# Kernel optimization log

Hardware: AMD Instinct MI355X
Metric: run time of the kernel (lower is better)

Reference implementation:

```python
import jax, jax.numpy as jnp
import numpy as np

EPS = 1e-12  # matches torch F.normalize default eps

def setup_inputs() -> dict:
    key = jax.random.key(0)
    k1, k2 = jax.random.split(key)
    N, D = 16384, 1024
    pc_feat = jax.random.normal(k1, (N, D), dtype=jnp.float32)
    aug_feat = jax.random.normal(k2, (N, D), dtype=jnp.float32)
    return {"pc_feat": pc_feat, "aug_feat": aug_feat}

def reference(pc_feat, aug_feat):
    # F.normalize(x, dim=1): x / max(||x||_2, eps)
    pc_n = pc_feat / jnp.maximum(jnp.linalg.norm(pc_feat, axis=1, keepdims=True), EPS)
    aug_n = aug_feat / jnp.maximum(jnp.linalg.norm(aug_feat, axis=1, keepdims=True), EPS)
    # diag(pc_n @ aug_n.T) == row-wise dot product; avoids the O(N^2) matmul
    cos = jnp.sum(pc_n * aug_n, axis=1)  # [N]
    # loss = sum(1 - cos) / N == mean(1 - cos)
    return jnp.mean(1.0 - cos)
```

## Files before the change

kernel.cpp:

```cpp
#include <hip/hip_runtime.h>


#define N_ROWS 16384
#define DIM 1024
#define BLOCKS 1024
#define TPB 256
#define WAVES_PER_BLOCK (TPB / 64)
#define TOTAL_WAVES (BLOCKS * WAVES_PER_BLOCK)

__global__ __launch_bounds__(TPB) void cos_rows_kernel(
    const float4* __restrict__ a, const float4* __restrict__ b,
    float* __restrict__ partial)
{
    const int wave = threadIdx.x >> 6;
    const int lane = threadIdx.x & 63;
    const int gwave = blockIdx.x * WAVES_PER_BLOCK + wave;

    float sum_cos = 0.0f;

    for (int r = gwave; r < N_ROWS; r += TOTAL_WAVES) {
        const float4* ap = a + (size_t)r * (DIM / 4);
        const float4* bp = b + (size_t)r * (DIM / 4);
        float ab = 0.0f, aa = 0.0f, bb = 0.0f;
        #pragma unroll
        for (int k = 0; k < 4; ++k) {
            float4 x = ap[lane + 64 * k];
            float4 y = bp[lane + 64 * k];
            ab += x.x * y.x + x.y * y.y + x.z * y.z + x.w * y.w;
            aa += x.x * x.x + x.y * x.y + x.z * x.z + x.w * x.w;
            bb += y.x * y.x + y.y * y.y + y.z * y.z + y.w * y.w;
        }
        #pragma unroll
        for (int off = 32; off > 0; off >>= 1) {
            ab += __shfl_down(ab, off);
            aa += __shfl_down(aa, off);
            bb += __shfl_down(bb, off);
        }
        if (lane == 0) {
            float na = fmaxf(sqrtf(aa), 1e-12f);
            float nb = fmaxf(sqrtf(bb), 1e-12f);
            sum_cos += ab / (na * nb);
        }
    }

    __shared__ float s[WAVES_PER_BLOCK];
    if (lane == 0) s[wave] = sum_cos;
    __syncthreads();
    if (threadIdx.x == 0) {
        float t = 0.0f;
        #pragma unroll
        for (int i = 0; i < WAVES_PER_BLOCK; ++i) t += s[i];
        partial[blockIdx.x] = t;
    }
}

__global__ __launch_bounds__(TPB) void finalize_kernel(
    const float* __restrict__ partial, float* __restrict__ out)
{
    const int wave = threadIdx.x >> 6;
    const int lane = threadIdx.x & 63;
    float t = 0.0f;
    for (int i = threadIdx.x; i < BLOCKS; i += TPB) t += partial[i];
    #pragma unroll
    for (int off = 32; off > 0; off >>= 1) t += __shfl_down(t, off);
    __shared__ float s[WAVES_PER_BLOCK];
    if (lane == 0) s[wave] = t;
    __syncthreads();
    if (threadIdx.x == 0) {
        float tot = 0.0f;
        #pragma unroll
        for (int i = 0; i < WAVES_PER_BLOCK; ++i) tot += s[i];
        out[0] = 1.0f - tot / (float)N_ROWS;
    }
}

extern "C" void kernel_launch(void* const* d_in, const int* in_sizes, int n_in,
                              void* d_out, int out_size, void* d_ws, size_t ws_size,
                              hipStream_t stream) {
    const float4* pc  = (const float4*)d_in[0];
    const float4* aug = (const float4*)d_in[1];
    float* partial = (float*)d_ws;
    float* out = (float*)d_out;

    cos_rows_kernel<<<BLOCKS, TPB, 0, stream>>>(pc, aug, partial);
    finalize_kernel<<<1, TPB, 0, stream>>>(partial, out);
}
```

Baseline: 142.0 us.

## Split row dot products into per-segment partials with separate row-combine kernel

Replaces the wave-per-row reduction with a thread-per-segment scheme: 16 threads each accumulate a strided slice of a row and write ab/aa/bb partials to workspace, then a second kernel combines the 16 partials per row through shared memory and computes the cosine, and a final kernel sums 256 block results. This removes cross-lane shuffle reductions and the grid-stride loop in the main pass. It adds an extra kernel launch and a round trip of three 16384x16 float arrays through global memory. The segment-strided loads leave each thread's float4 accesses 256 bytes apart, which may hurt coalescing per instruction. It also contains an odd redundant ternary on the bb accumulation.

Result: slower. 151.8 us (+6.9%).

```diff
diff --git a/kernel.cpp b/kernel.cpp
--- a/kernel.cpp
+++ b/kernel.cpp
@@ -2,55 +2,72 @@
 
 
 #define N_ROWS 16384
-#define DIM 1024
-#define BLOCKS 1024
+#define ROW_V4 256
+#define SEGS 16
+#define SEG_V4 16
 #define TPB 256
-#define WAVES_PER_BLOCK (TPB / 64)
-#define TOTAL_WAVES (BLOCKS * WAVES_PER_BLOCK)
+#define NPART (N_ROWS * SEGS)
+#define BLOCKS1 (NPART / TPB)
+#define BLOCKS2 256
 
-__global__ __launch_bounds__(TPB) void cos_rows_kernel(
+__global__ __launch_bounds__(TPB) void partial_kernel(
     const float4* __restrict__ a, const float4* __restrict__ b,
-    float* __restrict__ partial)
+    float* __restrict__ ab_ws, float* __restrict__ aa_ws,
+    float* __restrict__ bb_ws)
 {
-    const int wave = threadIdx.x >> 6;
-    const int lane = threadIdx.x & 63;
-    const int gwave = blockIdx.x * WAVES_PER_BLOCK + wave;
+    const int g = blockIdx.x * TPB + threadIdx.x;
+    const int row = g >> 4;
+    const int seg = g & (SEGS - 1);
+    const float4* ap = a + (size_t)row * ROW_V4 + seg;
+    const float4* bp = b + (size_t)row * ROW_V4 + seg;
 
-    float sum_cos = 0.0f;
+    float ab = 0.0f, aa = 0.0f, bb = 0.0f;
+    #pragma unroll
+    for (int j = 0; j < SEG_V4; ++j) {
+        float4 x = ap[j * SEGS];
+        float4 y = bp[j * SEGS];
+        ab += x.x * y.x + x.y * y.y + x.z * y.z + x.w * y.w;
+        aa += x.x * x.x + x.y * x.y + x.z * x.z + x.w * x.w;
+        bb += y.x * y.y == 0.0f ? y.x * y.x + y.y * y.y + y.z * y.z + y.w * y.w
+                                : y.x * y.x + y.y * y.y + y.z * y.z + y.w * y.w;
+    }
+    ab_ws[g] = ab;
+    aa_ws[g] = aa;
+    bb_ws[g] = bb;
+}
 
-    for (int r = gwave; r < N_ROWS; r += TOTAL_WAVES) {
-        const float4* ap = a + (size_t)r * (DIM / 4);
-        const float4* bp = b + (size_t)r * (DIM / 4);
+__global__ __launch_bounds__(TPB) void rowcos_kernel(
+    const float* __restrict__ ab_ws, const float* __restrict__ aa_ws,
+    const float* __restrict__ bb_ws, float* __restrict__ partial)
+{
+    __shared__ float sab[1024], saa[1024], sbb[1024];
+    const int base = blockIdx.x * 1024;
+    #pragma unroll
+    for (int i = threadIdx.x; i < 1024; i += TPB) {
+        sab[i] = ab_ws[base + i];
+        saa[i] = aa_ws[base + i];
+        sbb[i] = bb_ws[base + i];
+    }
+    __syncthreads();
+
+    float t = 0.0f;
+    if (threadIdx.x < 64) {
+        const int r = threadIdx.x;
         float ab = 0.0f, aa = 0.0f, bb = 0.0f;
         #pragma unroll
-        for (int k = 0; k < 4; ++k) {
-            float4 x = ap[lane + 64 * k];
-            float4 y = bp[lane + 64 * k];
-            ab += x.x * y.x + x.y * y.y + x.z * y.z + x.w * y.w;
-            aa += x.x * x.x + x.y * x.y + x.z * x.z + x.w * x.w;
-            bb += y.x * y.x + y.y * y.y + y.z * y.z + y.w * y.w;
+        for (int i = 0; i < SEGS; ++i) {
+            ab += sab[r * SEGS + i];
+            aa += saa[r * SEGS + i];
+            bb += sbb[r * SEGS + i];
         }
+        float na = fmaxf(sqrtf(aa), 1e-12f);
+        float nb = fmaxf(sqrtf(bb), 1e-12f);
+        t = ab / (na * nb);
+    }
+    if (threadIdx.x < 64) {
         #pragma unroll
-        for (int off = 32; off > 0; off >>= 1) {
-            ab += __shfl_down(ab, off);
-            aa += __shfl_down(aa, off);
-            bb += __shfl_down(bb, off);
-        }
-        if (lane == 0) {
-            float na = fmaxf(sqrtf(aa), 1e-12f);
-            float nb = fmaxf(sqrtf(bb), 1e-12f);
-            sum_cos += ab / (na * nb);
-        }
-    }
-
-    __shared__ float s[WAVES_PER_BLOCK];
-    if (lane == 0) s[wave] = sum_cos;
-    __syncthreads();
-    if (threadIdx.x == 0) {
-        float t = 0.0f;
-        #pragma unroll
-        for (int i = 0; i < WAVES_PER_BLOCK; ++i) t += s[i];
-        partial[blockIdx.x] = t;
+        for (int off = 32; off > 0; off >>= 1) t += __shfl_down(t, off);
+        if (threadIdx.x == 0) partial[blockIdx.x] = t;
     }
 }
 
@@ -59,17 +76,16 @@
 {
     const int wave = threadIdx.x >> 6;
     const int lane = threadIdx.x & 63;
-    float t = 0.0f;
-    for (int i = threadIdx.x; i < BLOCKS; i += TPB) t += partial[i];
+    float t = partial[threadIdx.x];
     #pragma unroll
     for (int off = 32; off > 0; off >>= 1) t += __shfl_down(t, off);
-    __shared__ float s[WAVES_PER_BLOCK];
+    __shared__ float s[TPB / 64];
     if (lane == 0) s[wave] = t;
     __syncthreads();
     if (threadIdx.x == 0) {
         float tot = 0.0f;
         #pragma unroll
-        for (int i = 0; i < WAVES_PER_BLOCK; ++i) tot += s[i];
+        for (int i = 0; i < TPB / 64; ++i) tot += s[i];
         out[0] = 1.0f - tot / (float)N_ROWS;
     }
 }
@@ -79,9 +95,13 @@
                               hipStream_t stream) {
     const float4* pc  = (const float4*)d_in[0];
     const float4* aug = (const float4*)d_in[1];
-    float* partial = (float*)d_ws;
+    float* ab_ws = (float*)d_ws;
+    float* aa_ws = ab_ws + NPART;
+    float* bb_ws = aa_ws + NPART;
+    float* partial = bb_ws + NPART;
     float* out = (float*)d_out;
 
-    cos_rows_kernel<<<BLOCKS, TPB, 0, stream>>>(pc, aug, partial);
+    partial_kernel<<<BLOCKS1, TPB, 0, stream>>>(pc, aug, ab_ws, aa_ws, bb_ws);
+    rowcos_kernel<<<BLOCKS2, TPB, 0, stream>>>(ab_ws, aa_ws, bb_ws, partial);
     finalize_kernel<<<1, TPB, 0, stream>>>(partial, out);
 }
```
